# Kernel optimization log

Hardware: AMD Instinct MI355X
Metric: run time of the kernel (lower is better)

Reference implementation:

```python
import jax, jax.numpy as jnp
import numpy as np


def _conv_relu(x, w, b):
    # keras Conv2D: NHWC input, HWIO kernel, VALID padding, stride 1, relu
    y = jax.lax.conv_general_dilated(
        x, w, window_strides=(1, 1), padding='VALID',
        dimension_numbers=('NHWC', 'HWIO', 'NHWC'))
    return jax.nn.relu(y + b)


def _maxpool2(x):
    # keras MaxPooling2D((2,2)): window 2x2, stride 2, VALID
    return jax.lax.reduce_window(
        x, -jnp.inf, jax.lax.max,
        window_dimensions=(1, 2, 2, 1), window_strides=(1, 2, 2, 1),
        padding='VALID')


def setup_inputs() -> dict:
    key = jax.random.key(0)
    ks = jax.random.split(key, 8)
    B = 4096
    return {
        'x': jax.random.normal(ks[0], (B, 14, 14, 1), jnp.float32),
        'conv1_w': jax.random.normal(ks[1], (3, 3, 1, 32), jnp.float32) * 0.1,
        'conv1_b': jnp.zeros((32,), jnp.float32),
        'conv2_w': jax.random.normal(ks[2], (3, 3, 32, 64), jnp.float32) * 0.05,
        'conv2_b': jnp.zeros((64,), jnp.float32),
        # trainable grid, initialized as tf.linspace(0,1,grid_size=50)
        'grid': jnp.linspace(0.0, 1.0, 50, dtype=jnp.float32),
        # KANLayer splines: output_dim=128 weights, each (input_dim=256, grid_size=50)
        'kan1_w': jax.random.normal(ks[3], (128, 256, 50), jnp.float32) * 0.05,
        # SimplifiedKANLayer splines: output_dim=64 weights, each (input_dim=128,)
        'kan2_w': jax.random.normal(ks[4], (64, 128), jnp.float32) * 0.05,
        'dense_w': jax.random.normal(ks[5], (64, 10), jnp.float32) * 0.05,
        'dense_b': jnp.zeros((10,), jnp.float32),
    }


def reference(x, conv1_w, conv1_b, conv2_w, conv2_b, grid, kan1_w, kan2_w,
              dense_w, dense_b):
    h = _conv_relu(x, conv1_w, conv1_b)   # (B,12,12,32)
    h = _maxpool2(h)                      # (B,6,6,32)
    h = _conv_relu(h, conv2_w, conv2_b)   # (B,4,4,64)
    h = _maxpool2(h)                      # (B,2,2,64)
    B = h.shape[0]
    h = h.reshape(B, -1)                  # (B,256) keras Flatten order (H,W,C)
    # KANLayer: linear hat basis relu(1-|x-g|) per (feature,grid), contracted
    # against per-output coefficients: out[b,o] = sum_{d,g} W[o,d,g]*basis[b,d,g]
    basis = jax.nn.relu(1.0 - jnp.abs(h[:, :, None] - grid[None, None, :]))  # (B,256,50)
    h = jnp.einsum('bdg,odg->bo', basis, kan1_w)  # (B,128)
    # SimplifiedKANLayer: out[b,o] = sum_d W2[o,d]*relu(h[b,d])
    h = jnp.einsum('bd,od->bo', jax.nn.relu(h), kan2_w)  # (B,64)
    return jax.nn.softmax(h @ dense_w + dense_b, axis=-1)  # (B,10)
```

## Files before the change

kernel.cpp:

```cpp
#include <hip/hip_runtime.h>
#include <hip/hip_bf16.h>
#include <hip/hip_fp16.h>

typedef float v2f __attribute__((ext_vector_type(2)));
typedef _Float16 f16x8 __attribute__((ext_vector_type(8)));
typedef float f32x4 __attribute__((ext_vector_type(4)));

__global__ __launch_bounds__(256) void k_prep(
    const float* __restrict__ kan1_w, const float* __restrict__ w2,
    const float* __restrict__ kan2_w, __half* __restrict__ tabN,
    _Float16* __restrict__ w2f, __half2* __restrict__ w2t) {
  __shared__ float wsh[128][51];
  int bid = blockIdx.x;
  int t = threadIdx.x;
  if (bid < 1024) {
    int d = bid >> 2;
    int q = bid & 3;
#pragma unroll
    for (int i = t; i < 128 * 50; i += 256) {
      int oo = i / 50;
      int g = i - oo * 50;
      wsh[oo][g] = kan1_w[(size_t)oo * 12800 + (size_t)d * 50 + g];
    }
    __syncthreads();
    int o = t & 127;
    int jh = t >> 7;
    const float* wr = &wsh[o][0];
    __half* trow = tabN + (size_t)d * 197 * 128 + o;
    const float inv98 = 1.0f / 98.0f;
    int ci = q * 2 + jh;
    int k0 = (ci * 98) >> 3;
    int k1 = ((ci + 1) * 98) >> 3;
    float lowW = 0.f, lowG = 0.f, highW = 0.f, highG = 0.f;
    {
      int gl0 = k0 - 48 > 0 ? k0 - 48 : 0;
      int gl1 = k0 < 49 ? k0 : 49;
      for (int g = gl0; g <= gl1; ++g) {
        float w = wr[g], gg = (float)g * (1.0f / 49.0f);
        lowW += w; lowG += w * gg;
      }
      for (int g = k0 + 1; g < 50; ++g) {
        float w = wr[g], gg = (float)g * (1.0f / 49.0f);
        highW += w; highG += w * gg;
      }
    }
    for (int k = k0; k < k1; ++k) {
      float A = highW - lowW;
      float Bc = (lowW + highW) + lowG - highG;
      float c0 = (float)(2 * k) * inv98 + 0.5f * inv98;
      float c1 = c0 + inv98;
      trow[(size_t)(2 * k) * 128] = __float2half(fmaf(A, c0, Bc));
      trow[(size_t)(2 * k + 1) * 128] = __float2half(fmaf(A, c1, Bc));
      if (k + 1 <= 49) {
        float wg = wr[k + 1], gg = (float)(k + 1) * (1.0f / 49.0f);
        lowW += wg; lowG += wg * gg;
        highW -= wg; highG -= wg * gg;
      }
      if (k >= 48) {
        float wg = wr[k - 48], gg = (float)(k - 48) * (1.0f / 49.0f);
        lowW -= wg; lowG -= wg * gg;
      }
    }
    if (ci == 7) trow[(size_t)196 * 128] = __float2half(0.f);
    return;
  }
  if (bid < 1096) {
    int i = (bid - 1024) * 256 + t;
    int n = i & 63;
    int row = i >> 6;
    int ci = row & 31;
    int tap = row >> 5;
    w2f[((tap * 4 + (ci >> 3)) * 64 + n) * 8 + (ci & 7)] = (_Float16)w2[i];
    return;
  }
  {
    int i = (bid - 1096) * 256 + t;
    int dp = i >> 6;
    int o = i & 63;
    w2t[i] = __floats2half2_rn(kan2_w[o * 128 + 2 * dp],
                               kan2_w[o * 128 + 2 * dp + 1]);
  }
}

#define NBC 4

__global__ __launch_bounds__(256)
__attribute__((amdgpu_waves_per_eu(2, 4))) void k_main(
    const float* __restrict__ x, const float* __restrict__ w1,
    const float* __restrict__ b1, const _Float16* __restrict__ w2f,
    const float* __restrict__ b2, const __half* __restrict__ tabN,
    const __half2* __restrict__ w2t, const float* __restrict__ dense_w,
    const float* __restrict__ dense_b, float* __restrict__ out) {
  __shared__ __align__(16) char sm1[4864];
  __shared__ __align__(16) char sm2[11520];
  float* xs = (float*)sm1;
  float* w1s = xs + NBC * 224;
  float* b1s = w1s + 288;
  unsigned short* meta = (unsigned short*)sm1;
  _Float16* h1l = (_Float16*)sm2;
  float* vs = (float*)sm2;
  float* us = vs + NBC * 128;
  float* ls = us + NBC * 64;
  int t = threadIdx.x;
  int bid = blockIdx.x;
  int b0 = bid * NBC;
  {
    for (int i = t; i < NBC * 224; i += 256) {
      int blb = i / 224;
      int rem = i - blb * 224;
      int r = rem >> 4;
      int cc = rem & 15;
      xs[i] = (cc < 14) ? x[(size_t)(b0 + blb) * 196 + r * 14 + cc] : 0.f;
    }
    for (int i = t; i < 288; i += 256) w1s[i] = w1[i];
    if (t < 32) b1s[t] = b1[t];
  }
  __syncthreads();
  int p = t >> 6;
  int c = t & 63;
  {
    int ch = c & 31;
    int half = c >> 5;
    float wr[9];
#pragma unroll
    for (int j = 0; j < 9; ++j) wr[j] = w1s[j * 32 + ch];
    float bias = b1s[ch];
    int y0 = 3 * half;
    const float* xb = xs + p * 224;
    _Float16* hrow = h1l + p * 1440 + ch;
#pragma unroll
    for (int yy = 0; yy < 3; ++yy) {
      int y = y0 + yy;
      float xr[4][16];
#pragma unroll
      for (int r = 0; r < 4; ++r) {
        float4* dstp = (float4*)xr[r];
        const float4* srcp = (const float4*)(xb + (2 * y + r) * 16);
#pragma unroll
        for (int q = 0; q < 4; ++q) dstp[q] = srcp[q];
      }
#pragma unroll
      for (int xx = 0; xx < 6; ++xx) {
        float m = -1e30f;
#pragma unroll
        for (int py = 0; py < 2; ++py)
#pragma unroll
          for (int px = 0; px < 2; ++px) {
            float s = 0.f;
#pragma unroll
            for (int dy = 0; dy < 3; ++dy)
#pragma unroll
              for (int dx = 0; dx < 3; ++dx)
                s = fmaf(xr[py + dy][2 * xx + px + dx], wr[dy * 3 + dx], s);
            m = fmaxf(m, s);
          }
        hrow[(y * 6 + xx) * 40] = (_Float16)fmaxf(m + bias, 0.f);
      }
    }
  }
  __syncthreads();
  {
    int lm = c & 15;
    int lk = c >> 4;
    int mbase = (lm >> 2) * 6 + (lm & 3);
    f32x4 acc[4];
#pragma unroll
    for (int nt = 0; nt < 4; ++nt) acc[nt] = (f32x4){0.f, 0.f, 0.f, 0.f};
    const _Float16* h0 = &h1l[p * 1440 + lk * 8];
#pragma unroll
    for (int tap = 0; tap < 9; ++tap) {
      int tapoff = (tap / 3) * 6 + (tap % 3);
      int po = (mbase + tapoff) * 40;
      f16x8 a0 = *(const f16x8*)(h0 + po);
      const _Float16* wb = &w2f[((tap * 4 + lk) * 64 + lm) * 8];
      f16x8 bf0 = *(const f16x8*)(wb);
      f16x8 bf1 = *(const f16x8*)(wb + 128);
      f16x8 bf2 = *(const f16x8*)(wb + 256);
      f16x8 bf3 = *(const f16x8*)(wb + 384);
      acc[0] = __builtin_amdgcn_mfma_f32_16x16x32_f16(a0, bf0, acc[0], 0, 0, 0);
      acc[1] = __builtin_amdgcn_mfma_f32_16x16x32_f16(a0, bf1, acc[1], 0, 0, 0);
      acc[2] = __builtin_amdgcn_mfma_f32_16x16x32_f16(a0, bf2, acc[2], 0, 0, 0);
      acc[3] = __builtin_amdgcn_mfma_f32_16x16x32_f16(a0, bf3, acc[3], 0, 0, 0);
    }
    float bias[4];
#pragma unroll
    for (int nt = 0; nt < 4; ++nt) bias[nt] = b2[nt * 16 + lm];
#pragma unroll
    for (int nt = 0; nt < 4; ++nt) {
      f32x4 A = acc[nt];
      float m01 = fmaxf(A.x, A.y);
      float m23 = fmaxf(A.z, A.w);
      m01 = fmaxf(m01, __shfl_xor(m01, 16));
      m23 = fmaxf(m23, __shfl_xor(m23, 16));
      float val = (lk & 1) ? m23 : m01;
      val = fmaxf(val + bias[nt], 0.f);
      int d = lk * 64 + nt * 16 + lm;
      int k = (int)(val * 98.0f);
      k = k > 196 ? 196 : k;
      meta[d * NBC + p] = (unsigned short)(d * 197 + k);
    }
  }
  __syncthreads();
  {
    int lq = c >> 4;
    int lo = c & 15;
    int phase0 = bid & 7;
    v2f acc[4];
#pragma unroll
    for (int e = 0; e < 4; ++e) acc[e] = (v2f){0.f, 0.f};
    int offs[2][8];
    float4 raws[2][8];
    {
      int d0 = (phase0 & 7) << 5;
#pragma unroll
      for (int dq = 0; dq < 8; ++dq)
        offs[0][dq] = ((int)meta[(d0 + 4 * dq + lq) * NBC + p]) << 7;
#pragma unroll
      for (int dq = 0; dq < 8; ++dq)
        raws[0][dq] = *(const float4*)(tabN + offs[0][dq] + lo * 8);
    }
#pragma unroll
    for (int ph = 0; ph < 8; ++ph) {
      const int cur = ph & 1, nxt = cur ^ 1;
      if (ph < 7) {
        int d0n = ((phase0 + ph + 1) & 7) << 5;
#pragma unroll
        for (int dq = 0; dq < 8; ++dq)
          offs[nxt][dq] = ((int)meta[(d0n + 4 * dq + lq) * NBC + p]) << 7;
#pragma unroll
        for (int dq = 0; dq < 8; ++dq)
          raws[nxt][dq] = *(const float4*)(tabN + offs[nxt][dq] + lo * 8);
      }
      __half2 hs[4];
#pragma unroll
      for (int e = 0; e < 4; ++e) hs[e] = __builtin_bit_cast(__half2, 0u);
#pragma unroll
      for (int dq = 0; dq < 8; ++dq) {
        hs[0] = __hadd2(hs[0], __builtin_bit_cast(__half2, raws[cur][dq].x));
        hs[1] = __hadd2(hs[1], __builtin_bit_cast(__half2, raws[cur][dq].y));
        hs[2] = __hadd2(hs[2], __builtin_bit_cast(__half2, raws[cur][dq].z));
        hs[3] = __hadd2(hs[3], __builtin_bit_cast(__half2, raws[cur][dq].w));
      }
#pragma unroll
      for (int e = 0; e < 4; ++e) {
        float2 f = __half22float2(hs[e]);
        acc[e].x += f.x;
        acc[e].y += f.y;
      }
    }
#pragma unroll
    for (int e = 0; e < 4; ++e) {
      acc[e].x += __shfl_xor(acc[e].x, 16);
      acc[e].y += __shfl_xor(acc[e].y, 16);
      acc[e].x += __shfl_xor(acc[e].x, 32);
      acc[e].y += __shfl_xor(acc[e].y, 32);
    }
    if (lq == 0) {
      float* vp = vs + p * 128 + lo * 8;
      *(float4*)vp = make_float4(fmaxf(acc[0].x, 0.f), fmaxf(acc[0].y, 0.f),
                                 fmaxf(acc[1].x, 0.f), fmaxf(acc[1].y, 0.f));
      *(float4*)(vp + 4) =
          make_float4(fmaxf(acc[2].x, 0.f), fmaxf(acc[2].y, 0.f),
                      fmaxf(acc[3].x, 0.f), fmaxf(acc[3].y, 0.f));
    }
  }
  __syncthreads();
  {
    float a = 0.f;
    const float* v0 = vs + p * 128;
#pragma unroll 8
    for (int dp = 0; dp < 64; ++dp) {
      float2 wf = __half22float2(w2t[dp * 64 + c]);
      float2 vq = *(const float2*)(v0 + 2 * dp);
      a = fmaf(wf.x, vq.x, a);
      a = fmaf(wf.y, vq.y, a);
    }
    us[p * 64 + c] = a;
  }
  __syncthreads();
  if (t < NBC * 10) {
    int b = t / 10;
    int j = t - b * 10;
    float s = dense_b[j];
    for (int k2 = 0; k2 < 64; ++k2)
      s = fmaf(us[b * 64 + k2], dense_w[k2 * 10 + j], s);
    ls[b * 12 + j] = s;
  }
  __syncthreads();
  if (t < NBC) {
    int b = t;
    float m = -1e30f;
#pragma unroll
    for (int j = 0; j < 10; ++j) m = fmaxf(m, ls[b * 12 + j]);
    float e[10];
    float sum = 0.f;
#pragma unroll
    for (int j = 0; j < 10; ++j) {
      e[j] = __expf(ls[b * 12 + j] - m);
      sum += e[j];
    }
    float inv = 1.0f / sum;
#pragma unroll
    for (int j = 0; j < 10; ++j) out[(size_t)(b0 + b) * 10 + j] = e[j] * inv;
  }
}

extern "C" void kernel_launch(void* const* d_in, const int* in_sizes, int n_in,
                              void* d_out, int out_size, void* d_ws, size_t ws_size,
                              hipStream_t stream) {
  const float* x      = (const float*)d_in[0];
  const float* w1     = (const float*)d_in[1];
  const float* b1     = (const float*)d_in[2];
  const float* w2     = (const float*)d_in[3];
  const float* b2     = (const float*)d_in[4];
  const float* kan1_w = (const float*)d_in[6];
  const float* kan2_w = (const float*)d_in[7];
  const float* dw     = (const float*)d_in[8];
  const float* db     = (const float*)d_in[9];
  float* out = (float*)d_out;
  int B = in_sizes[0] / 196;

  char* wsb = (char*)d_ws;
  __half* tabN = (__half*)wsb;
  size_t off1 = (size_t)256 * 197 * 128 * sizeof(__half);
  off1 = (off1 + 255) & ~(size_t)255;
  _Float16* w2f = (_Float16*)(wsb + off1);
  size_t off2 = off1 + 18432 * sizeof(_Float16);
  off2 = (off2 + 255) & ~(size_t)255;
  __half2* w2t = (__half2*)(wsb + off2);

  k_prep<<<dim3(1112), dim3(256), 0, stream>>>(kan1_w, w2, kan2_w, tabN, w2f, w2t);
  k_main<<<dim3(B / NBC), dim3(256), 0, stream>>>(
      x, w1, b1, w2f, b2, tabN, w2t, dw, db, out);
}
```

Before: 111.4 us.

## Split fused main kernel into conv, table-gather, and tail kernels

Breaks the single fused kernel into three launches. The conv stage writes per-sample table indices to global memory. A gather kernel partitions the 256 features into 8 slices so each block reads one slice of the table for 32 samples, which is meant to improve cache locality of the large fp16 lookup table. A tail kernel sums the 8 partial results and runs the remaining layers. In exchange it adds two launches and global round trips for the index buffer and the 8x partial sums (about 16 MB of fp32 traffic).

```diff
diff --git a/kernel.cpp b/kernel.cpp
--- a/kernel.cpp
+++ b/kernel.cpp
@@ -5,6 +5,8 @@
 typedef float v2f __attribute__((ext_vector_type(2)));
 typedef _Float16 f16x8 __attribute__((ext_vector_type(8)));
 typedef float f32x4 __attribute__((ext_vector_type(4)));
+
+#define NBC 4
 
 __global__ __launch_bounds__(256) void k_prep(
     const float* __restrict__ kan1_w, const float* __restrict__ w2,
@@ -82,25 +84,17 @@
   }
 }
 
-#define NBC 4
-
 __global__ __launch_bounds__(256)
-__attribute__((amdgpu_waves_per_eu(2, 4))) void k_main(
+__attribute__((amdgpu_waves_per_eu(2, 4))) void k_conv(
     const float* __restrict__ x, const float* __restrict__ w1,
     const float* __restrict__ b1, const _Float16* __restrict__ w2f,
-    const float* __restrict__ b2, const __half* __restrict__ tabN,
-    const __half2* __restrict__ w2t, const float* __restrict__ dense_w,
-    const float* __restrict__ dense_b, float* __restrict__ out) {
+    const float* __restrict__ b2, unsigned short* __restrict__ metaG) {
   __shared__ __align__(16) char sm1[4864];
   __shared__ __align__(16) char sm2[11520];
   float* xs = (float*)sm1;
   float* w1s = xs + NBC * 224;
   float* b1s = w1s + 288;
-  unsigned short* meta = (unsigned short*)sm1;
   _Float16* h1l = (_Float16*)sm2;
-  float* vs = (float*)sm2;
-  float* us = vs + NBC * 128;
-  float* ls = us + NBC * 64;
   int t = threadIdx.x;
   int bid = blockIdx.x;
   int b0 = bid * NBC;
@@ -197,74 +191,73 @@
       int d = lk * 64 + nt * 16 + lm;
       int k = (int)(val * 98.0f);
       k = k > 196 ? 196 : k;
-      meta[d * NBC + p] = (unsigned short)(d * 197 + k);
-    }
-  }
-  __syncthreads();
-  {
-    int lq = c >> 4;
-    int lo = c & 15;
-    int phase0 = bid & 7;
-    v2f acc[4];
-#pragma unroll
-    for (int e = 0; e < 4; ++e) acc[e] = (v2f){0.f, 0.f};
-    int offs[2][8];
-    float4 raws[2][8];
-    {
-      int d0 = (phase0 & 7) << 5;
-#pragma unroll
-      for (int dq = 0; dq < 8; ++dq)
-        offs[0][dq] = ((int)meta[(d0 + 4 * dq + lq) * NBC + p]) << 7;
-#pragma unroll
-      for (int dq = 0; dq < 8; ++dq)
-        raws[0][dq] = *(const float4*)(tabN + offs[0][dq] + lo * 8);
-    }
-#pragma unroll
-    for (int ph = 0; ph < 8; ++ph) {
-      const int cur = ph & 1, nxt = cur ^ 1;
-      if (ph < 7) {
-        int d0n = ((phase0 + ph + 1) & 7) << 5;
-#pragma unroll
-        for (int dq = 0; dq < 8; ++dq)
-          offs[nxt][dq] = ((int)meta[(d0n + 4 * dq + lq) * NBC + p]) << 7;
-#pragma unroll
-        for (int dq = 0; dq < 8; ++dq)
-          raws[nxt][dq] = *(const float4*)(tabN + offs[nxt][dq] + lo * 8);
-      }
-      __half2 hs[4];
-#pragma unroll
-      for (int e = 0; e < 4; ++e) hs[e] = __builtin_bit_cast(__half2, 0u);
-#pragma unroll
-      for (int dq = 0; dq < 8; ++dq) {
-        hs[0] = __hadd2(hs[0], __builtin_bit_cast(__half2, raws[cur][dq].x));
-        hs[1] = __hadd2(hs[1], __builtin_bit_cast(__half2, raws[cur][dq].y));
-        hs[2] = __hadd2(hs[2], __builtin_bit_cast(__half2, raws[cur][dq].z));
-        hs[3] = __hadd2(hs[3], __builtin_bit_cast(__half2, raws[cur][dq].w));
-      }
-#pragma unroll
-      for (int e = 0; e < 4; ++e) {
-        float2 f = __half22float2(hs[e]);
-        acc[e].x += f.x;
-        acc[e].y += f.y;
-      }
-    }
-#pragma unroll
-    for (int e = 0; e < 4; ++e) {
-      acc[e].x += __shfl_xor(acc[e].x, 16);
-      acc[e].y += __shfl_xor(acc[e].y, 16);
-      acc[e].x += __shfl_xor(acc[e].x, 32);
-      acc[e].y += __shfl_xor(acc[e].y, 32);
-    }
-    if (lq == 0) {
-      float* vp = vs + p * 128 + lo * 8;
-      *(float4*)vp = make_float4(fmaxf(acc[0].x, 0.f), fmaxf(acc[0].y, 0.f),
-                                 fmaxf(acc[1].x, 0.f), fmaxf(acc[1].y, 0.f));
-      *(float4*)(vp + 4) =
-          make_float4(fmaxf(acc[2].x, 0.f), fmaxf(acc[2].y, 0.f),
-                      fmaxf(acc[3].x, 0.f), fmaxf(acc[3].y, 0.f));
-    }
-  }
-  __syncthreads();
+      metaG[(size_t)(b0 + p) * 256 + d] = (unsigned short)(d * 197 + k);
+    }
+  }
+}
+
+__global__ __launch_bounds__(256) void k_gather(
+    const __half* __restrict__ tabN, const unsigned short* __restrict__ metaG,
+    float* __restrict__ partialG, int B) {
+  __shared__ unsigned short ms[32][32];
+  int bid = blockIdx.x;
+  int t = threadIdx.x;
+  int s = bid & 7;
+  int gid = bid >> 3;
+  int b0 = gid * 32;
+  {
+    unsigned int* mdst = (unsigned int*)&ms[0][0];
+    for (int j = t; j < 512; j += 256) {
+      int row = j >> 4, col = j & 15;
+      mdst[j] = *(const unsigned int*)(metaG + (size_t)(b0 + row) * 256 +
+                                       s * 32 + col * 2);
+    }
+  }
+  __syncthreads();
+  int w = t >> 6;
+  int l = t & 63;
+  for (int bb = 0; bb < 8; ++bb) {
+    int brow = w * 8 + bb;
+    float ax = 0.f, ay = 0.f;
+#pragma unroll
+    for (int ch = 0; ch < 4; ++ch) {
+      __half2 hsum = __builtin_bit_cast(__half2, 0u);
+#pragma unroll
+      for (int dd = 0; dd < 8; ++dd) {
+        int off = ((int)ms[brow][ch * 8 + dd]) << 7;
+        hsum = __hadd2(hsum, *(const __half2*)(tabN + off + 2 * l));
+      }
+      float2 f = __half22float2(hsum);
+      ax += f.x;
+      ay += f.y;
+    }
+    *(float2*)(partialG + ((size_t)s * B + (b0 + brow)) * 128 + 2 * l) =
+        make_float2(ax, ay);
+  }
+}
+
+__global__ __launch_bounds__(256) void k_tail(
+    const float* __restrict__ partialG, const __half2* __restrict__ w2t,
+    const float* __restrict__ dense_w, const float* __restrict__ dense_b,
+    float* __restrict__ out, int B) {
+  __shared__ float vs[NBC * 128];
+  __shared__ float us[NBC * 64];
+  __shared__ float ls[NBC * 12];
+  int t = threadIdx.x;
+  int bid = blockIdx.x;
+  int b0 = bid * NBC;
+  for (int i = t; i < NBC * 128; i += 256) {
+    int bb = i >> 7;
+    int o = i & 127;
+    float sum = 0.f;
+#pragma unroll
+    for (int s = 0; s < 8; ++s)
+      sum += partialG[((size_t)s * B + (b0 + bb)) * 128 + o];
+    vs[i] = fmaxf(sum, 0.f);
+  }
+  __syncthreads();
+  int p = t >> 6;
+  int c = t & 63;
   {
     float a = 0.f;
     const float* v0 = vs + p * 128;
@@ -328,8 +321,15 @@
   size_t off2 = off1 + 18432 * sizeof(_Float16);
   off2 = (off2 + 255) & ~(size_t)255;
   __half2* w2t = (__half2*)(wsb + off2);
+  size_t off3 = off2 + 4096 * sizeof(__half2);
+  off3 = (off3 + 255) & ~(size_t)255;
+  unsigned short* metaG = (unsigned short*)(wsb + off3);
+  size_t off4 = off3 + (size_t)B * 256 * sizeof(unsigned short);
+  off4 = (off4 + 255) & ~(size_t)255;
+  float* partialG = (float*)(wsb + off4);
 
   k_prep<<<dim3(1112), dim3(256), 0, stream>>>(kan1_w, w2, kan2_w, tabN, w2f, w2t);
-  k_main<<<dim3(B / NBC), dim3(256), 0, stream>>>(
-      x, w1, b1, w2f, b2, tabN, w2t, dw, db, out);
-}
+  k_conv<<<dim3(B / NBC), dim3(256), 0, stream>>>(x, w1, b1, w2f, b2, metaG);
+  k_gather<<<dim3(8 * (B / 32)), dim3(256), 0, stream>>>(tabN, metaG, partialG, B);
+  k_tail<<<dim3(B / NBC), dim3(256), 0, stream>>>(partialG, w2t, dw, db, out, B);
+}
```

After: 124.4 us. 11.6% more time.
